# Performance work log

Measured on AMD Instinct MI355X. Metric: run time of the kernel, lower is better.

## Reference

```python
import math
import jax, jax.numpy as jnp
import numpy as np

EPS_BOUND = 1e-06  # Consts.Eps, used by LowerBound on temperature


def setup_inputs() -> dict:
    key = jax.random.key(0)
    k1, k2 = jax.random.split(key)
    x = jax.random.normal(k1, (8, 128, 16, 16), dtype=jnp.float32)
    codebook = jax.random.normal(k2, (4, 4096, 32), dtype=jnp.float32)
    temperature = jnp.ones((4, 1, 1, 1), dtype=jnp.float32)
    return {"x": x, "codebook": codebook, "temperature": temperature}


def _distance(x, codebook):
    m, k, d = codebook.shape
    n, _, h, w = x.shape
    xr = x.reshape(n, m, d, h, w)
    x2 = (xr ** 2).sum(2)[:, :, None]                  # (n,m,1,h,w)
    c2 = (codebook ** 2).sum(-1)[:, :, None, None]     # (m,k,1,1)
    inter = jnp.einsum('nmdhw,mkd->nmkhw', xr, codebook)
    dist = x2 + c2 - 2.0 * inter                        # (n,m,k,h,w)
    return dist.transpose(0, 1, 3, 4, 2)                # (n,m,h,w,k)


def reference(x, codebook, temperature):
    m, k, d = codebook.shape
    scale = math.sqrt(k)
    # logit = -distance / sqrt(k), scaled by LowerBound(temperature)
    logit = (-_distance(x, codebook) / scale) * jnp.maximum(temperature, EPS_BOUND)
    # hard gumbel-softmax with tau=1.0 (straight-through)
    eps = jnp.finfo(logit.dtype).eps
    u = jnp.clip(jax.random.uniform(jax.random.key(42), logit.shape, logit.dtype),
                 eps, 1.0 - eps)
    gumbels = -jnp.log(-jnp.log(u))
    y_soft = jax.nn.softmax(logit + gumbels, axis=-1)
    hard_idx = jnp.argmax(y_soft, axis=-1)
    y_hard = jax.nn.one_hot(hard_idx, k, dtype=logit.dtype)
    sample = y_hard - jax.lax.stop_gradient(y_soft) + y_soft
    # permutationRate = 0.0 -> _permute is identity
    code = jnp.argmax(logit, axis=-1)                   # (n,m,h,w)
    one_hot = jax.nn.one_hot(code, k, dtype=logit.dtype)
    return sample, code, one_hot, logit
```

## Files before the change

### kernel.cpp

```cpp
#include <hip/hip_runtime.h>
#include <stdint.h>


typedef short bf16x8 __attribute__((ext_vector_type(8)));
typedef float f32x4  __attribute__((ext_vector_type(4)));
typedef float floatx4 __attribute__((ext_vector_type(4)));

__device__ __forceinline__ uint32_t rotl32(uint32_t x, uint32_t r){
  return (x << r) | (x >> (32u - r));
}

__device__ __forceinline__ float gumbel_from_e(uint32_t e){
  uint32_t x0 = 0u, x1 = e;
  const uint32_t ks0 = 0u, ks1 = 42u, ks2 = 0x1BD11BF0u;
  x0 += ks0; x1 += ks1;
#define TFR4(a,b,c,d2) \
  x0 += x1; x1 = rotl32(x1,(a)); x1 ^= x0; \
  x0 += x1; x1 = rotl32(x1,(b)); x1 ^= x0; \
  x0 += x1; x1 = rotl32(x1,(c)); x1 ^= x0; \
  x0 += x1; x1 = rotl32(x1,(d2)); x1 ^= x0;
  TFR4(13,15,26,6)  x0 += ks1; x1 += ks2 + 1u;
  TFR4(17,29,16,24) x0 += ks2; x1 += ks0 + 2u;
  TFR4(13,15,26,6)  x0 += ks0; x1 += ks1 + 3u;
  TFR4(17,29,16,24) x0 += ks1; x1 += ks2 + 4u;
  TFR4(13,15,26,6)  x0 += ks2; x1 += ks0 + 5u;
#undef TFR4
  uint32_t bits = x0 ^ x1;
  float u = __uint_as_float((bits >> 9) | 0x3F800000u) - 1.0f;
  u = fminf(fmaxf(u, 1.1920929e-07f), __uint_as_float(0x3F7FFFFEu));
  const float LN2 = 0.69314718055994531f;
  float v = -LN2 * __log2f(u);
  return -LN2 * __log2f(v);
}

__device__ __forceinline__ void split_bf16(float v, unsigned short& hi, unsigned short& lo){
  uint32_t b = __float_as_uint(v);
  hi = (unsigned short)(b >> 16);
  float r = v - __uint_as_float(b & 0xFFFF0000u);
  lo = (unsigned short)(__float_as_uint(r) >> 16);
}

template<bool USE_WS>
__global__ __launch_bounds__(512, 8) void k_logits(
    const float* __restrict__ x, const float* __restrict__ cb,
    const float* __restrict__ temp, float* __restrict__ logit_out,
    float* __restrict__ sample, float* __restrict__ onehot,
    float* __restrict__ part_ws){
  __shared__ __align__(16) char smem[38016];
  unsigned short* cbh = (unsigned short*)smem;
  unsigned short* cbl = cbh + 8192;
  unsigned short* xbh = cbl + 8192;
  unsigned short* xbl = xbh + 1024;
  float* c2l = (float*)(xbl + 1024);
  float* x2l = c2l + 256;
  float* red = (float*)smem;

  const int tid = threadIdx.x;
  const int b = blockIdx.x;
  const int kt = b & 15;
  const int rt = (b >> 4) & 63;
  const int m  = b >> 10;
  const int n  = rt >> 3;
  const int hw0 = (rt & 7) << 5;
  const int k0 = kt << 8;
  const int rowbase = ((n << 2) + m) * 256 + hw0;

  const float* xm = x + ((n * 128 + m * 32) * 256 + hw0);
  #pragma unroll
  for (int i = 0; i < 2; ++i){
    int idx = tid + (i << 9);
    int d = idx >> 5, r = idx & 31;
    float v = xm[(d << 8) + r];
    unsigned short h, l;
    split_bf16(v, h, l);
    xbh[(r << 5) + d] = h;
    xbl[(r << 5) + d] = l;
  }
  const float4* cb4 = (const float4*)(cb + (m * 131072 + k0 * 32));
  #pragma unroll
  for (int i = 0; i < 4; ++i){
    int f = tid + (i << 9);
    float4 v = cb4[f];
    int kk = f >> 3, dq = f & 7;
    unsigned short h0,h1,h2,h3,l0,l1,l2,l3;
    split_bf16(v.x, h0, l0); split_bf16(v.y, h1, l1);
    split_bf16(v.z, h2, l2); split_bf16(v.w, h3, l3);
    uint2 hw_, lw_;
    hw_.x = (uint32_t)h0 | ((uint32_t)h1 << 16);
    hw_.y = (uint32_t)h2 | ((uint32_t)h3 << 16);
    lw_.x = (uint32_t)l0 | ((uint32_t)l1 << 16);
    lw_.y = (uint32_t)l2 | ((uint32_t)l3 << 16);
    *(uint2*)&cbh[(kk << 5) + (dq << 2)] = hw_;
    *(uint2*)&cbl[(kk << 5) + (dq << 2)] = lw_;
    float p = fmaf(v.x, v.x, fmaf(v.y, v.y, fmaf(v.z, v.z, v.w * v.w)));
    p += __shfl_xor(p, 1);
    p += __shfl_xor(p, 2);
    p += __shfl_xor(p, 4);
    if (dq == 0) c2l[kk] = p;
  }
  __syncthreads();

  if (tid < 32){
    float s = 0.f;
    #pragma unroll
    for (int d = 0; d < 32; ++d){
      float vh = __uint_as_float(((uint32_t)xbh[(tid << 5) + d]) << 16);
      float vl = __uint_as_float(((uint32_t)xbl[(tid << 5) + d]) << 16);
      float v = vh + vl;
      s = fmaf(v, v, s);
    }
    x2l[tid] = s;
  }
  __syncthreads();

  const int lane = tid & 63;
  const int w    = tid >> 6;
  const int mh   = w >> 2;
  const int ng   = w & 3;
  const int l15  = lane & 15;
  const int kgrp = lane >> 4;

  bf16x8 Ah = *(const bf16x8*)&xbh[((mh * 16 + l15) << 5) + (kgrp << 3)];
  bf16x8 Al = *(const bf16x8*)&xbl[((mh * 16 + l15) << 5) + (kgrp << 3)];

  float x2r[4];
  #pragma unroll
  for (int j = 0; j < 4; ++j) x2r[j] = x2l[mh * 16 + (kgrp << 2) + j];

  const float tcl = fmaxf(temp[m], 1e-6f);
  const floatx4 z4 = (floatx4)(0.f);
  float bl[4], bg[4]; int bli[4], bgi[4];
  #pragma unroll
  for (int j = 0; j < 4; ++j){ bl[j] = -INFINITY; bg[j] = -INFINITY; bli[j] = 0; bgi[j] = 0; }

  #pragma unroll
  for (int t = 0; t < 4; ++t){
    const int nt = (ng << 2) + t;
    const int k_blk = (nt << 4) + l15;
    bf16x8 Bh = *(const bf16x8*)&cbh[(k_blk << 5) + (kgrp << 3)];
    bf16x8 Bl = *(const bf16x8*)&cbl[(k_blk << 5) + (kgrp << 3)];
    f32x4 acc = {0.f, 0.f, 0.f, 0.f};
    acc = __builtin_amdgcn_mfma_f32_16x16x32_bf16(Ah, Bh, acc, 0, 0, 0);
    acc = __builtin_amdgcn_mfma_f32_16x16x32_bf16(Ah, Bl, acc, 0, 0, 0);
    acc = __builtin_amdgcn_mfma_f32_16x16x32_bf16(Al, Bh, acc, 0, 0, 0);

    const float c2 = c2l[k_blk];
    const int k_g = k0 + k_blk;
    #pragma unroll
    for (int j = 0; j < 4; ++j){
      const int r_blk = mh * 16 + (kgrp << 2) + j;
      const int row_g = rowbase + r_blk;
      float dist = x2r[j] + c2 - 2.0f * acc[j];
      float lgt = (-dist) * 0.015625f * tcl;
      __builtin_nontemporal_store(lgt, &logit_out[((size_t)row_g << 12) + k_g]);
      float lg = lgt + gumbel_from_e(((uint32_t)row_g << 12) + (uint32_t)k_g);
      if (lgt > bl[j]) { bl[j] = lgt; bli[j] = k_g; }
      if (lg  > bg[j]) { bg[j] = lg;  bgi[j] = k_g; }
    }

    if (USE_WS){
      int s = tid + (t << 9);
      int r2 = s >> 6, w4 = s & 63;
      size_t f4 = (((size_t)(rowbase + r2)) << 10) + (k0 >> 2) + w4;
      __builtin_nontemporal_store(z4, (floatx4*)onehot + f4);
      __builtin_nontemporal_store(z4, (floatx4*)sample + f4);
    }
  }

  __syncthreads();
  #pragma unroll
  for (int j = 0; j < 4; ++j){
    int row = mh * 16 + (kgrp << 2) + j;
    int slot = (ng << 4) + l15;
    red[        row * 65 + slot] = bl[j];
    red[2080 +  row * 65 + slot] = __int_as_float(bli[j]);
    red[4160 +  row * 65 + slot] = bg[j];
    red[6240 +  row * 65 + slot] = __int_as_float(bgi[j]);
  }
  __syncthreads();
  if (tid < 64){
    const int r = tid & 31;
    const bool doG = (tid >= 32);
    const int off_v = doG ? 4160 : 0;
    const int off_i = doG ? 6240 : 2080;
    float bv = -INFINITY; int bi = 0;
    for (int g2 = 0; g2 < 64; ++g2){
      float v = red[off_v + r * 65 + g2];
      int  ix = __float_as_int(red[off_i + r * 65 + g2]);
      if (v > bv || (v == bv && ix < bi)){ bv = v; bi = ix; }
    }
    const int row_g = rowbase + r;
    if (USE_WS){
      *(float2*)&part_ws[((size_t)row_g << 6) + (kt << 2) + (doG ? 2 : 0)]
          = make_float2(bv, __int_as_float(bi));
    } else {
      float* part = sample + ((size_t)row_g << 12);
      part[(doG ? 32 : 0)  + kt] = bv;
      part[(doG ? 48 : 16) + kt] = __int_as_float(bi);
    }
  }

  if (!USE_WS){
    const float4 zz = make_float4(0.f, 0.f, 0.f, 0.f);
    #pragma unroll
    for (int i2 = 0; i2 < 4; ++i2){
      int s = tid + (i2 << 9);
      int r = s >> 6, w4 = s & 63;
      size_t f4 = (((size_t)(rowbase + r)) << 10) + (k0 >> 2) + w4;
      ((float4*)onehot)[f4] = zz;
      if (!(kt == 0 && w4 < 16))
        ((float4*)sample)[f4] = zz;
    }
  }
}

template<bool USE_WS>
__global__ __launch_bounds__(256) void k_finalize(
    float* __restrict__ sample, float* __restrict__ code_out,
    float* __restrict__ onehot, const float* __restrict__ part_ws){
  const int tid = threadIdx.x;
  const int row = (blockIdx.x << 2) + (tid >> 6);
  const int lane = tid & 63;
  float* srow = sample + ((size_t)row << 12);
  float* orow = onehot + ((size_t)row << 12);

  const int g = (lane >> 4) & 1;
  const int l16 = lane & 15;
  float v; int ix;
  if (lane < 32){
    if (USE_WS){
      float2 p2 = *(const float2*)&part_ws[((size_t)row << 6) + (l16 << 2) + (g ? 2 : 0)];
      v = p2.x; ix = __float_as_int(p2.y);
    } else {
      v  = srow[g * 32 + l16];
      ix = __float_as_int(srow[g * 32 + 16 + l16]);
    }
  } else { v = -INFINITY; ix = 0x7fffffff; }
  #pragma unroll
  for (int off = 1; off < 16; off <<= 1){
    float ov = __shfl_xor(v, off, 16);
    int   oi = __shfl_xor(ix, off, 16);
    if (ov > v || (ov == v && oi < ix)){ v = ov; ix = oi; }
  }
  const int codei = __shfl(ix, 0, 64);
  const int hard  = __shfl(ix, 16, 64);

  if (USE_WS){
    if (lane == 0)      srow[hard]  = 1.0f;
    else if (lane == 1) orow[codei] = 1.0f;
    else if (lane == 2) code_out[row] = (float)codei;
  } else {
    if (lane < 16){
      float4 vs = make_float4(0.f, 0.f, 0.f, 0.f);
      if ((hard >> 2) == lane) ((float*)&vs)[hard & 3] = 1.0f;
      ((float4*)srow)[lane] = vs;
    } else if (lane == 16){
      if (hard >= 64) srow[hard] = 1.0f;
    } else if (lane == 17){
      orow[codei] = 1.0f;
    } else if (lane == 18){
      code_out[row] = (float)codei;
    }
  }
}

extern "C" void kernel_launch(void* const* d_in, const int* in_sizes, int n_in,
                              void* d_out, int out_size, void* d_ws, size_t ws_size,
                              hipStream_t stream) {
  const float* x    = (const float*)d_in[0];
  const float* cb   = (const float*)d_in[1];
  const float* temp = (const float*)d_in[2];
  float* out    = (float*)d_out;
  float* sample = out;
  float* code   = out + 33554432;
  float* onehot = code + 8192;
  float* logit  = onehot + 33554432;
  float* ws     = (float*)d_ws;

  const bool use_ws = ws_size >= (size_t)8192 * 64 * sizeof(float);
  if (use_ws){
    hipLaunchKernelGGL((k_logits<true>), dim3(4096), dim3(512), 0, stream,
                       x, cb, temp, logit, sample, onehot, ws);
    hipLaunchKernelGGL((k_finalize<true>), dim3(2048), dim3(256), 0, stream,
                       sample, code, onehot, ws);
  } else {
    hipLaunchKernelGGL((k_logits<false>), dim3(4096), dim3(512), 0, stream,
                       x, cb, temp, logit, sample, onehot, ws);
    hipLaunchKernelGGL((k_finalize<false>), dim3(2048), dim3(256), 0, stream,
                       sample, code, onehot, ws);
  }
}
```

Baseline: 112.0 us.

## Process two codebook k-tiles per block to reuse the x tile and halve partials

Each logits block now loops over two consecutive 256-wide k-tiles instead of one. The x tile load, its bf16 split and the x² computation happen once per block, and the grid shrinks from 4096 to 2048 blocks. Per-row argmax partials drop from 16 to 8, so the finalize kernel's reduction is narrowed to match. The cost is an extra barrier between the two codebook tiles and less block-level parallelism, on a kernel dominated by large output writes.

```diff
diff --git a/kernel.cpp b/kernel.cpp
--- a/kernel.cpp
+++ b/kernel.cpp
@@ -57,12 +57,11 @@
 
   const int tid = threadIdx.x;
   const int b = blockIdx.x;
-  const int kt = b & 15;
-  const int rt = (b >> 4) & 63;
-  const int m  = b >> 10;
-  const int n  = rt >> 3;
+  const int ktp = b & 7;
+  const int rt  = (b >> 3) & 63;
+  const int m   = b >> 9;
+  const int n   = rt >> 3;
   const int hw0 = (rt & 7) << 5;
-  const int k0 = kt << 8;
   const int rowbase = ((n << 2) + m) * 256 + hw0;
 
   const float* xm = x + ((n * 128 + m * 32) * 256 + hw0);
@@ -76,42 +75,6 @@
     xbh[(r << 5) + d] = h;
     xbl[(r << 5) + d] = l;
   }
-  const float4* cb4 = (const float4*)(cb + (m * 131072 + k0 * 32));
-  #pragma unroll
-  for (int i = 0; i < 4; ++i){
-    int f = tid + (i << 9);
-    float4 v = cb4[f];
-    int kk = f >> 3, dq = f & 7;
-    unsigned short h0,h1,h2,h3,l0,l1,l2,l3;
-    split_bf16(v.x, h0, l0); split_bf16(v.y, h1, l1);
-    split_bf16(v.z, h2, l2); split_bf16(v.w, h3, l3);
-    uint2 hw_, lw_;
-    hw_.x = (uint32_t)h0 | ((uint32_t)h1 << 16);
-    hw_.y = (uint32_t)h2 | ((uint32_t)h3 << 16);
-    lw_.x = (uint32_t)l0 | ((uint32_t)l1 << 16);
-    lw_.y = (uint32_t)l2 | ((uint32_t)l3 << 16);
-    *(uint2*)&cbh[(kk << 5) + (dq << 2)] = hw_;
-    *(uint2*)&cbl[(kk << 5) + (dq << 2)] = lw_;
-    float p = fmaf(v.x, v.x, fmaf(v.y, v.y, fmaf(v.z, v.z, v.w * v.w)));
-    p += __shfl_xor(p, 1);
-    p += __shfl_xor(p, 2);
-    p += __shfl_xor(p, 4);
-    if (dq == 0) c2l[kk] = p;
-  }
-  __syncthreads();
-
-  if (tid < 32){
-    float s = 0.f;
-    #pragma unroll
-    for (int d = 0; d < 32; ++d){
-      float vh = __uint_as_float(((uint32_t)xbh[(tid << 5) + d]) << 16);
-      float vl = __uint_as_float(((uint32_t)xbl[(tid << 5) + d]) << 16);
-      float v = vh + vl;
-      s = fmaf(v, v, s);
-    }
-    x2l[tid] = s;
-  }
-  __syncthreads();
 
   const int lane = tid & 63;
   const int w    = tid >> 6;
@@ -120,50 +83,103 @@
   const int l15  = lane & 15;
   const int kgrp = lane >> 4;
 
-  bf16x8 Ah = *(const bf16x8*)&xbh[((mh * 16 + l15) << 5) + (kgrp << 3)];
-  bf16x8 Al = *(const bf16x8*)&xbl[((mh * 16 + l15) << 5) + (kgrp << 3)];
-
-  float x2r[4];
-  #pragma unroll
-  for (int j = 0; j < 4; ++j) x2r[j] = x2l[mh * 16 + (kgrp << 2) + j];
-
   const float tcl = fmaxf(temp[m], 1e-6f);
   const floatx4 z4 = (floatx4)(0.f);
+  bf16x8 Ah, Al;
+  float x2r[4];
   float bl[4], bg[4]; int bli[4], bgi[4];
   #pragma unroll
   for (int j = 0; j < 4; ++j){ bl[j] = -INFINITY; bg[j] = -INFINITY; bli[j] = 0; bgi[j] = 0; }
 
   #pragma unroll
-  for (int t = 0; t < 4; ++t){
-    const int nt = (ng << 2) + t;
-    const int k_blk = (nt << 4) + l15;
-    bf16x8 Bh = *(const bf16x8*)&cbh[(k_blk << 5) + (kgrp << 3)];
-    bf16x8 Bl = *(const bf16x8*)&cbl[(k_blk << 5) + (kgrp << 3)];
-    f32x4 acc = {0.f, 0.f, 0.f, 0.f};
-    acc = __builtin_amdgcn_mfma_f32_16x16x32_bf16(Ah, Bh, acc, 0, 0, 0);
-    acc = __builtin_amdgcn_mfma_f32_16x16x32_bf16(Ah, Bl, acc, 0, 0, 0);
-    acc = __builtin_amdgcn_mfma_f32_16x16x32_bf16(Al, Bh, acc, 0, 0, 0);
-
-    const float c2 = c2l[k_blk];
-    const int k_g = k0 + k_blk;
+  for (int ki = 0; ki < 2; ++ki){
+    const int kt = (ktp << 1) + ki;
+    const int k0 = kt << 8;
+    if (ki > 0) __syncthreads();
+
+    const float4* cb4 = (const float4*)(cb + (m * 131072 + k0 * 32));
     #pragma unroll
-    for (int j = 0; j < 4; ++j){
-      const int r_blk = mh * 16 + (kgrp << 2) + j;
-      const int row_g = rowbase + r_blk;
-      float dist = x2r[j] + c2 - 2.0f * acc[j];
-      float lgt = (-dist) * 0.015625f * tcl;
-      __builtin_nontemporal_store(lgt, &logit_out[((size_t)row_g << 12) + k_g]);
-      float lg = lgt + gumbel_from_e(((uint32_t)row_g << 12) + (uint32_t)k_g);
-      if (lgt > bl[j]) { bl[j] = lgt; bli[j] = k_g; }
-      if (lg  > bg[j]) { bg[j] = lg;  bgi[j] = k_g; }
-    }
-
-    if (USE_WS){
-      int s = tid + (t << 9);
-      int r2 = s >> 6, w4 = s & 63;
-      size_t f4 = (((size_t)(rowbase + r2)) << 10) + (k0 >> 2) + w4;
-      __builtin_nontemporal_store(z4, (floatx4*)onehot + f4);
-      __builtin_nontemporal_store(z4, (floatx4*)sample + f4);
+    for (int i = 0; i < 4; ++i){
+      int f = tid + (i << 9);
+      float4 v = cb4[f];
+      int kk = f >> 3, dq = f & 7;
+      unsigned short h0,h1,h2,h3,l0,l1,l2,l3;
+      split_bf16(v.x, h0, l0); split_bf16(v.y, h1, l1);
+      split_bf16(v.z, h2, l2); split_bf16(v.w, h3, l3);
+      uint2 hw_, lw_;
+      hw_.x = (uint32_t)h0 | ((uint32_t)h1 << 16);
+      hw_.y = (uint32_t)h2 | ((uint32_t)h3 << 16);
+      lw_.x = (uint32_t)l0 | ((uint32_t)l1 << 16);
+      lw_.y = (uint32_t)l2 | ((uint32_t)l3 << 16);
+      *(uint2*)&cbh[(kk << 5) + (dq << 2)] = hw_;
+      *(uint2*)&cbl[(kk << 5) + (dq << 2)] = lw_;
+      float p = fmaf(v.x, v.x, fmaf(v.y, v.y, fmaf(v.z, v.z, v.w * v.w)));
+      p += __shfl_xor(p, 1);
+      p += __shfl_xor(p, 2);
+      p += __shfl_xor(p, 4);
+      if (dq == 0) c2l[kk] = p;
+    }
+    __syncthreads();
+
+    if (ki == 0){
+      if (tid < 32){
+        float s = 0.f;
+        #pragma unroll
+        for (int d = 0; d < 32; ++d){
+          float vh = __uint_as_float(((uint32_t)xbh[(tid << 5) + d]) << 16);
+          float vl = __uint_as_float(((uint32_t)xbl[(tid << 5) + d]) << 16);
+          float v = vh + vl;
+          s = fmaf(v, v, s);
+        }
+        x2l[tid] = s;
+      }
+      __syncthreads();
+      Ah = *(const bf16x8*)&xbh[((mh * 16 + l15) << 5) + (kgrp << 3)];
+      Al = *(const bf16x8*)&xbl[((mh * 16 + l15) << 5) + (kgrp << 3)];
+      #pragma unroll
+      for (int j = 0; j < 4; ++j) x2r[j] = x2l[mh * 16 + (kgrp << 2) + j];
+    }
+
+    #pragma unroll
+    for (int t = 0; t < 4; ++t){
+      const int nt = (ng << 2) + t;
+      const int k_blk = (nt << 4) + l15;
+      bf16x8 Bh = *(const bf16x8*)&cbh[(k_blk << 5) + (kgrp << 3)];
+      bf16x8 Bl = *(const bf16x8*)&cbl[(k_blk << 5) + (kgrp << 3)];
+      f32x4 acc = {0.f, 0.f, 0.f, 0.f};
+      acc = __builtin_amdgcn_mfma_f32_16x16x32_bf16(Ah, Bh, acc, 0, 0, 0);
+      acc = __builtin_amdgcn_mfma_f32_16x16x32_bf16(Ah, Bl, acc, 0, 0, 0);
+      acc = __builtin_amdgcn_mfma_f32_16x16x32_bf16(Al, Bh, acc, 0, 0, 0);
+
+      const float c2 = c2l[k_blk];
+      const int k_g = k0 + k_blk;
+      #pragma unroll
+      for (int j = 0; j < 4; ++j){
+        const int r_blk = mh * 16 + (kgrp << 2) + j;
+        const int row_g = rowbase + r_blk;
+        float dist = x2r[j] + c2 - 2.0f * acc[j];
+        float lgt = (-dist) * 0.015625f * tcl;
+        __builtin_nontemporal_store(lgt, &logit_out[((size_t)row_g << 12) + k_g]);
+        float lg = lgt + gumbel_from_e(((uint32_t)row_g << 12) + (uint32_t)k_g);
+        if (lgt > bl[j]) { bl[j] = lgt; bli[j] = k_g; }
+        if (lg  > bg[j]) { bg[j] = lg;  bgi[j] = k_g; }
+      }
+
+      if (USE_WS){
+        int s = tid + (t << 9);
+        int r2 = s >> 6, w4 = s & 63;
+        size_t f4 = (((size_t)(rowbase + r2)) << 10) + (k0 >> 2) + w4;
+        __builtin_nontemporal_store(z4, (floatx4*)onehot + f4);
+        __builtin_nontemporal_store(z4, (floatx4*)sample + f4);
+      } else {
+        const float4 zz = make_float4(0.f, 0.f, 0.f, 0.f);
+        int s = tid + (t << 9);
+        int r2 = s >> 6, w4 = s & 63;
+        size_t f4 = (((size_t)(rowbase + r2)) << 10) + (k0 >> 2) + w4;
+        ((float4*)onehot)[f4] = zz;
+        if (!(kt == 0 && w4 < 16))
+          ((float4*)sample)[f4] = zz;
+      }
     }
   }
 
@@ -191,25 +207,12 @@
     }
     const int row_g = rowbase + r;
     if (USE_WS){
-      *(float2*)&part_ws[((size_t)row_g << 6) + (kt << 2) + (doG ? 2 : 0)]
+      *(float2*)&part_ws[((size_t)row_g << 6) + (ktp << 2) + (doG ? 2 : 0)]
           = make_float2(bv, __int_as_float(bi));
     } else {
       float* part = sample + ((size_t)row_g << 12);
-      part[(doG ? 32 : 0)  + kt] = bv;
-      part[(doG ? 48 : 16) + kt] = __int_as_float(bi);
-    }
-  }
-
-  if (!USE_WS){
-    const float4 zz = make_float4(0.f, 0.f, 0.f, 0.f);
-    #pragma unroll
-    for (int i2 = 0; i2 < 4; ++i2){
-      int s = tid + (i2 << 9);
-      int r = s >> 6, w4 = s & 63;
-      size_t f4 = (((size_t)(rowbase + r)) << 10) + (k0 >> 2) + w4;
-      ((float4*)onehot)[f4] = zz;
-      if (!(kt == 0 && w4 < 16))
-        ((float4*)sample)[f4] = zz;
+      part[(doG ? 32 : 0)  + ktp] = bv;
+      part[(doG ? 48 : 16) + ktp] = __int_as_float(bi);
     }
   }
 }
@@ -224,26 +227,26 @@
   float* srow = sample + ((size_t)row << 12);
   float* orow = onehot + ((size_t)row << 12);
 
-  const int g = (lane >> 4) & 1;
-  const int l16 = lane & 15;
+  const int g = (lane >> 3) & 1;
+  const int l8 = lane & 7;
   float v; int ix;
-  if (lane < 32){
+  if (lane < 16){
     if (USE_WS){
-      float2 p2 = *(const float2*)&part_ws[((size_t)row << 6) + (l16 << 2) + (g ? 2 : 0)];
+      float2 p2 = *(const float2*)&part_ws[((size_t)row << 6) + (l8 << 2) + (g ? 2 : 0)];
       v = p2.x; ix = __float_as_int(p2.y);
     } else {
-      v  = srow[g * 32 + l16];
-      ix = __float_as_int(srow[g * 32 + 16 + l16]);
+      v  = srow[g * 32 + l8];
+      ix = __float_as_int(srow[g * 32 + 16 + l8]);
     }
   } else { v = -INFINITY; ix = 0x7fffffff; }
   #pragma unroll
-  for (int off = 1; off < 16; off <<= 1){
-    float ov = __shfl_xor(v, off, 16);
-    int   oi = __shfl_xor(ix, off, 16);
+  for (int off = 1; off < 8; off <<= 1){
+    float ov = __shfl_xor(v, off, 8);
+    int   oi = __shfl_xor(ix, off, 8);
     if (ov > v || (ov == v && oi < ix)){ v = ov; ix = oi; }
   }
   const int codei = __shfl(ix, 0, 64);
-  const int hard  = __shfl(ix, 16, 64);
+  const int hard  = __shfl(ix, 8, 64);
 
   if (USE_WS){
     if (lane == 0)      srow[hard]  = 1.0f;
@@ -279,12 +282,12 @@
 
   const bool use_ws = ws_size >= (size_t)8192 * 64 * sizeof(float);
   if (use_ws){
-    hipLaunchKernelGGL((k_logits<true>), dim3(4096), dim3(512), 0, stream,
+    hipLaunchKernelGGL((k_logits<true>), dim3(2048), dim3(512), 0, stream,
                        x, cb, temp, logit, sample, onehot, ws);
     hipLaunchKernelGGL((k_finalize<true>), dim3(2048), dim3(256), 0, stream,
                        sample, code, onehot, ws);
   } else {
-    hipLaunchKernelGGL((k_logits<false>), dim3(4096), dim3(512), 0, stream,
+    hipLaunchKernelGGL((k_logits<false>), dim3(2048), dim3(512), 0, stream,
                        x, cb, temp, logit, sample, onehot, ws);
     hipLaunchKernelGGL((k_finalize<false>), dim3(2048), dim3(256), 0, stream,
                        sample, code, onehot, ws);
```

Result: slower. 154.1 us (+37.6%).
